# Performance work log

Measured on AMD Instinct MI355X. Metric: run time of the kernel, lower is better.

The kernel has to match this reference:

```python
import jax, jax.numpy as jnp
import numpy as np

N_NODES = 100000
N_EDGES = 1600000
D_IN = 128
H1 = 128           # hidden_channels
H2 = int(H1 * 0.6) # 76, per int(hidden_channels * 0.6)
D_OUT = 64


def setup_inputs() -> dict:
    key = jax.random.key(0)
    ks = jax.random.split(key, 12)
    def lin(k, fan_in, fan_out):
        # torch Linear default init: U(-1/sqrt(fan_in), 1/sqrt(fan_in)); stored as [in, out]
        bound = 1.0 / np.sqrt(fan_in)
        return jax.random.uniform(k, (fan_in, fan_out), jnp.float32, -bound, bound)
    x = jax.random.normal(ks[0], (N_NODES, D_IN), jnp.float32)
    edge_index = jax.random.randint(ks[1], (2, N_EDGES), 0, N_NODES, dtype=jnp.int64)
    return {
        "x": x,
        "edge_index": edge_index,
        "Wl1": lin(ks[2], D_IN, H1),  "Wr1": lin(ks[3], D_IN, H1),
        "b1": jnp.zeros((H1,), jnp.float32),
        "Wl2": lin(ks[4], H1, H2),    "Wr2": lin(ks[5], H1, H2),
        "b2": jnp.zeros((H2,), jnp.float32),
        "Wl3": lin(ks[6], H2, D_OUT), "Wr3": lin(ks[7], H2, D_OUT),
        "b3": jnp.zeros((D_OUT,), jnp.float32),
    }


def reference(x, edge_index, Wl1, Wr1, b1, Wl2, Wr2, b2, Wl3, Wr3, b3):
    src, dst = edge_index[0], edge_index[1]
    n = x.shape[0]
    # in-degree of each target node (mean aggregation denominator), clamped to 1
    deg = jax.ops.segment_sum(jnp.ones_like(src, dtype=x.dtype), dst, num_segments=n)
    inv_deg = (1.0 / jnp.maximum(deg, 1.0))[:, None]

    def sage(h, Wl, Wr, b):
        # gather source features, scatter-add to targets, mean, then dual linear
        agg = jax.ops.segment_sum(h[src], dst, num_segments=n) * inv_deg
        return agg @ Wl + h @ Wr + b  # lin_l(mean_j x_j) + lin_r(x_i) + bias

    h = jax.nn.relu(sage(x, Wl1, Wr1, b1))
    h = jax.nn.relu(sage(h, Wl2, Wr2, b2))
    return sage(h, Wl3, Wr3, b3)
```

## Files before the change

kernel.cpp:

```cpp
#include <hip/hip_runtime.h>
#include <hip/hip_bf16.h>
#include <cstdint>
#include <cstddef>


typedef __attribute__((ext_vector_type(8))) short bf16x8;
typedef __attribute__((ext_vector_type(4))) float f32x4;

__device__ __forceinline__ short f2bf(float f) {
  uint32_t u = __builtin_bit_cast(uint32_t, f);
  u += 0x7fffu + ((u >> 16) & 1u);
  return (short)(u >> 16);
}
__device__ __forceinline__ float bflo(uint32_t u) {
  union { uint32_t i; float f; } v; v.i = u << 16; return v.f;
}
__device__ __forceinline__ float bfhi(uint32_t u) {
  union { uint32_t i; float f; } v; v.i = u & 0xffff0000u; return v.f;
}
__device__ __forceinline__ uint32_t pkbf(float a, float b) {
  return (uint32_t)(uint16_t)f2bf(a) | ((uint32_t)(uint16_t)f2bf(b) << 16);
}

__global__ void k_detect(const int* __restrict__ ei, int* __restrict__ flag, int E) {
  int t = threadIdx.x;
  int stride = E / 4096; if (stride < 1) stride = 1;
  int found = 0;
  for (int i = t; i < 4096; i += 256) {
    long long e = (long long)i * stride;
    if (e < E && ei[2 * e + 1] != 0) found = 1;
  }
  if (found) atomicOr(flag, 1);
}

__device__ __forceinline__ int edge_val(const int* ei, int is64, size_t pos) {
  return is64 ? ei[2 * pos] : ei[pos];
}

#define GPART 256

__global__ __launch_bounds__(256)
void k_bhist(const int* __restrict__ ei, const int* __restrict__ flag,
             int* __restrict__ hist, int E, int NB, int CPB) {
  __shared__ int lh[1024];
  int g = blockIdx.x, t = threadIdx.x;
  for (int b = t; b < NB; b += 256) lh[b] = 0;
  __syncthreads();
  int is64 = (*flag == 0);
  int e0 = g * CPB, e1 = min(e0 + CPB, E);
  for (int e = e0 + t; e < e1; e += 256) {
    int d = edge_val(ei, is64, (size_t)E + e);
    atomicAdd(&lh[d >> 7], 1);
  }
  __syncthreads();
  for (int b = t; b < NB; b += 256) hist[(size_t)g * NB + b] = lh[b];
}

__global__ void k_csum(const int* __restrict__ hist, int* __restrict__ total,
                       int NB, int G) {
  int b = blockIdx.x, t = threadIdx.x;
  int s = 0;
  for (int g = t; g < G; g += 64) s += hist[(size_t)g * NB + b];
  for (int off = 32; off; off >>= 1) s += __shfl_down(s, off);
  if (t == 0) total[b] = s;
}

__global__ void k_bscan(const int* __restrict__ total, int* __restrict__ bbase,
                        int NB) {
  __shared__ int sh[1024];
  int t = threadIdx.x;
  int v = (t < NB) ? total[t] : 0;
  sh[t] = v; __syncthreads();
  for (int off = 1; off < 1024; off <<= 1) {
    int x = (t >= off) ? sh[t - off] : 0;
    __syncthreads();
    sh[t] += x;
    __syncthreads();
  }
  if (t < NB) bbase[t] = sh[t] - v;
  if (t == NB - 1) bbase[NB] = sh[t];
}

__global__ void k_coff(int* __restrict__ hist, const int* __restrict__ bbase,
                       int NB, int G) {
  int b = blockIdx.x, t = threadIdx.x;
  int carry = bbase[b];
  for (int g0 = 0; g0 < G; g0 += 64) {
    int v = hist[(size_t)(g0 + t) * NB + b];
    int incl = v;
    #pragma unroll
    for (int off = 1; off < 64; off <<= 1) {
      int x = __shfl_up(incl, off);
      if (t >= off) incl += x;
    }
    hist[(size_t)(g0 + t) * NB + b] = carry + incl - v;
    carry += __shfl(incl, 63);
  }
}

__global__ __launch_bounds__(256)
void k_bscatter(const int* __restrict__ ei, const int* __restrict__ flag,
                const int* __restrict__ off, uint32_t* __restrict__ staging,
                int E, int NB, int CPB) {
  __shared__ int lcur[1024];
  int g = blockIdx.x, t = threadIdx.x;
  for (int b = t; b < NB; b += 256) lcur[b] = off[(size_t)g * NB + b];
  __syncthreads();
  int is64 = (*flag == 0);
  int e0 = g * CPB, e1 = min(e0 + CPB, E);
  for (int e = e0 + t; e < e1; e += 256) {
    int s = edge_val(ei, is64, (size_t)e);
    int d = edge_val(ei, is64, (size_t)E + e);
    int p = atomicAdd(&lcur[d >> 7], 1);
    staging[p] = ((uint32_t)(d & 127) << 25) | (uint32_t)s;
  }
}

#define LDSCAP 12288
__global__ __launch_bounds__(256)
void k_bfinal(const uint32_t* __restrict__ staging, const int* __restrict__ bbase,
              int* __restrict__ row_start, int* __restrict__ sorted_src,
              int N, int NB, int E) {
  __shared__ uint32_t ent[LDSCAP];
  __shared__ int cnt[128];
  __shared__ int pre[128];
  int b = blockIdx.x, t = threadIdx.x;
  int base = bbase[b], sz = bbase[b + 1] - base;
  int n0 = b << 7;
  if (t < 128) cnt[t] = 0;
  __syncthreads();
  bool fit = (sz <= LDSCAP);
  if (fit) {
    for (int i = t; i < sz; i += 256) {
      uint32_t u = staging[base + i];
      ent[i] = u;
      atomicAdd(&cnt[u >> 25], 1);
    }
  } else {
    for (int i = t; i < sz; i += 256)
      atomicAdd(&cnt[staging[base + i] >> 25], 1);
  }
  __syncthreads();
  if (t < 128) pre[t] = cnt[t];
  __syncthreads();
  #pragma unroll
  for (int off = 1; off < 128; off <<= 1) {
    int x = (t < 128 && t >= off) ? pre[t - off] : 0;
    __syncthreads();
    if (t < 128) pre[t] += x;
    __syncthreads();
  }
  int nn = N - n0; if (nn > 128) nn = 128;
  if (t < 128) {
    int ex = pre[t] - cnt[t];
    if (t < nn) row_start[n0 + t] = base + ex;
    cnt[t] = ex;
  }
  if (b == NB - 1 && t == 0) row_start[N] = E;
  __syncthreads();
  if (fit) {
    for (int i = t; i < sz; i += 256) {
      uint32_t u = ent[i];
      int p = atomicAdd(&cnt[u >> 25], 1);
      sorted_src[base + p] = (int)(u & 0x1FFFFFFu);
    }
  } else {
    for (int i = t; i < sz; i += 256) {
      uint32_t u = staging[base + i];
      int p = atomicAdd(&cnt[u >> 25], 1);
      sorted_src[base + p] = (int)(u & 0x1FFFFFFu);
    }
  }
}

__global__ void k_wprep(const float* __restrict__ Wl, const float* __restrict__ Wr,
                        short* __restrict__ Wt, int K, int H, int Hp, int Kp, int NP) {
  int idx = blockIdx.x * 256 + threadIdx.x;
  if (idx >= NP * Kp) return;
  int c = idx / Kp, k = idx - c * Kp;
  float v = 0.f;
  if (k < K) {
    if (c < H) v = Wl[(size_t)k * H + c];
    else if (c >= Hp && c - Hp < H) v = Wr[(size_t)k * H + (c - Hp)];
  }
  Wt[idx] = f2bf(v);
}

template<int MODE, int NKS, int QBF16>
__global__ __launch_bounds__(256, 4)
void k_gemm2(const void* __restrict__ Av, const short* __restrict__ Wt,
             const float* __restrict__ bias, short* __restrict__ P,
             void* __restrict__ Qv, int M, int lda, int H, int Hp, int F) {
  const int Kp = NKS * 32;
  int t = threadIdx.x;
  int wv = t >> 6, lane = t & 63;
  int l16 = lane & 15, lk8 = (lane >> 4) * 8;
  int m0 = blockIdx.x * 64;
  int f0 = blockIdx.y * 8 + wv * 2;
  int nf = F - f0; nf = nf < 0 ? 0 : (nf > 2 ? 2 : nf);
  if (nf == 0) return;

  bf16x8 b[2][NKS];
  float4 bia[2];
  int cbase[2]; bool isPc[2]; bool cok[2];
  #pragma unroll
  for (int cf = 0; cf < 2; cf++) {
    int cfrag = f0 + cf;
    bool p = cfrag * 16 < Hp;
    int cb = cfrag * 16 + ((lane >> 4) << 2) - (p ? 0 : Hp);
    cbase[cf] = cb; isPc[cf] = p;
    cok[cf] = (cf < nf) && (cb < H);
    bia[cf] = make_float4(0.f, 0.f, 0.f, 0.f);
    if (cok[cf] && !p) bia[cf] = *(const float4*)(bias + cb);
    if (cf < nf) {
      const short* wp = Wt + (size_t)(cfrag * 16 + l16) * Kp + lk8;
      #pragma unroll
      for (int ks = 0; ks < NKS; ks++)
        b[cf][ks] = *(const bf16x8*)(wp + ks * 32);
    }
  }

  #pragma unroll
  for (int rf = 0; rf < 4; rf++) {
    int node = m0 + rf * 16 + l16;
    bool rok = node < M;
    bf16x8 a[NKS];
    if (MODE == 0) {
      const float* ap = (const float*)Av + (size_t)node * lda + lk8;
      #pragma unroll
      for (int ks = 0; ks < NKS; ks++) {
        if (rok) {
          float4 v0 = *(const float4*)(ap + ks * 32);
          float4 v1 = *(const float4*)(ap + ks * 32 + 4);
          bf16x8 r;
          r[0] = f2bf(v0.x); r[1] = f2bf(v0.y); r[2] = f2bf(v0.z); r[3] = f2bf(v0.w);
          r[4] = f2bf(v1.x); r[5] = f2bf(v1.y); r[6] = f2bf(v1.z); r[7] = f2bf(v1.w);
          a[ks] = r;
        } else {
          a[ks] = (bf16x8){0, 0, 0, 0, 0, 0, 0, 0};
        }
      }
    } else {
      const short* ap = (const short*)Av + (size_t)node * lda + lk8;
      #pragma unroll
      for (int ks = 0; ks < NKS; ks++)
        a[ks] = rok ? *(const bf16x8*)(ap + ks * 32)
                    : (bf16x8){0, 0, 0, 0, 0, 0, 0, 0};
    }

    f32x4 acc[2];
    acc[0] = (f32x4){0.f, 0.f, 0.f, 0.f};
    acc[1] = (f32x4){0.f, 0.f, 0.f, 0.f};
    #pragma unroll
    for (int ks = 0; ks < NKS; ks++) {
      #pragma unroll
      for (int cf = 0; cf < 2; cf++) {
        if (cf < nf)
          acc[cf] = __builtin_amdgcn_mfma_f32_16x16x32_bf16(b[cf][ks], a[ks], acc[cf], 0, 0, 0);
      }
    }

    if (rok) {
      #pragma unroll
      for (int cf = 0; cf < 2; cf++) {
        if (cok[cf]) {
          if (isPc[cf]) {
            uint2 pk;
            pk.x = pkbf(acc[cf][0], acc[cf][1]);
            pk.y = pkbf(acc[cf][2], acc[cf][3]);
            *(uint2*)(P + (size_t)node * H + cbase[cf]) = pk;
          } else if (QBF16) {
            uint2 pk;
            pk.x = pkbf(acc[cf][0] + bia[cf].x, acc[cf][1] + bia[cf].y);
            pk.y = pkbf(acc[cf][2] + bia[cf].z, acc[cf][3] + bia[cf].w);
            *(uint2*)((short*)Qv + (size_t)node * H + cbase[cf]) = pk;
          } else {
            float4 r;
            r.x = acc[cf][0] + bia[cf].x; r.y = acc[cf][1] + bia[cf].y;
            r.z = acc[cf][2] + bia[cf].z; r.w = acc[cf][3] + bia[cf].w;
            *(float4*)((float*)Qv + (size_t)node * H + cbase[cf]) = r;
          }
        }
      }
    }
  }
}

template<int RELU, int PACK, int OUTBF16, int QBF16>
__global__ __launch_bounds__(256)
void k_agg(const short* __restrict__ P, const void* Q,
           const int* __restrict__ rs, const int* __restrict__ srcs,
           void* out, int N, int H, int HSo) {
  int wave = threadIdx.x >> 6;
  int lane = threadIdx.x & 63;
  int node = blockIdx.x * 4 + wave;
  if (node >= N) return;
  int start = rs[node];
  int deg = rs[node + 1] - start;
  int c = lane * PACK;
  bool act = c < H;
  float a0 = 0.f, a1 = 0.f;
  const int* sp = srcs + start;

  for (int base = 0; base < deg; base += 64) {
    int cnt = deg - base; if (cnt > 64) cnt = 64;
    int myidx = (lane < cnt) ? sp[base + lane] : 0;
    int e = 0;
    int nfull = cnt & ~3;
    for (; e < nfull; e += 4) {
      int s0 = __shfl(myidx, e);
      int s1 = __shfl(myidx, e + 1);
      int s2 = __shfl(myidx, e + 2);
      int s3 = __shfl(myidx, e + 3);
      if (act) {
        if (PACK == 2) {
          uint32_t u0 = *(const uint32_t*)(P + (size_t)s0 * H + c);
          uint32_t u1 = *(const uint32_t*)(P + (size_t)s1 * H + c);
          uint32_t u2 = *(const uint32_t*)(P + (size_t)s2 * H + c);
          uint32_t u3 = *(const uint32_t*)(P + (size_t)s3 * H + c);
          a0 += bflo(u0); a1 += bfhi(u0);
          a0 += bflo(u1); a1 += bfhi(u1);
          a0 += bflo(u2); a1 += bfhi(u2);
          a0 += bflo(u3); a1 += bfhi(u3);
        } else {
          uint32_t u0 = *(const uint16_t*)(P + (size_t)s0 * H + c);
          uint32_t u1 = *(const uint16_t*)(P + (size_t)s1 * H + c);
          uint32_t u2 = *(const uint16_t*)(P + (size_t)s2 * H + c);
          uint32_t u3 = *(const uint16_t*)(P + (size_t)s3 * H + c);
          a0 += bflo(u0) + bflo(u1) + bflo(u2) + bflo(u3);
        }
      }
    }
    for (; e < cnt; ++e) {
      int s0 = __shfl(myidx, e);
      if (act) {
        if (PACK == 2) {
          uint32_t u0 = *(const uint32_t*)(P + (size_t)s0 * H + c);
          a0 += bflo(u0); a1 += bfhi(u0);
        } else {
          uint32_t u0 = *(const uint16_t*)(P + (size_t)s0 * H + c);
          a0 += bflo(u0);
        }
      }
    }
  }

  if (!act) return;
  float scale = 1.f / (float)(deg > 0 ? deg : 1);
  size_t oq = (size_t)node * H + c;
  size_t oo = (size_t)node * HSo + c;
  if (PACK == 2) {
    float q0, q1;
    if (QBF16) {
      uint32_t qu = *(const uint32_t*)((const short*)Q + oq);
      q0 = bflo(qu); q1 = bfhi(qu);
    } else {
      float2 q = *(const float2*)((const float*)Q + oq);
      q0 = q.x; q1 = q.y;
    }
    float v0 = a0 * scale + q0;
    float v1 = a1 * scale + q1;
    if (RELU) { v0 = fmaxf(v0, 0.f); v1 = fmaxf(v1, 0.f); }
    if (OUTBF16) {
      *(uint32_t*)((short*)out + oo) = pkbf(v0, v1);
    } else {
      float2 r; r.x = v0; r.y = v1;
      *(float2*)((float*)out + oo) = r;
    }
  } else {
    float q0;
    if (QBF16) q0 = bflo(*(const uint16_t*)((const short*)Q + oq));
    else       q0 = ((const float*)Q)[oq];
    float v0 = a0 * scale + q0;
    if (RELU) v0 = fmaxf(v0, 0.f);
    if (OUTBF16) ((short*)out)[oo] = f2bf(v0);
    else ((float*)out)[oo] = v0;
  }
}

extern "C" void kernel_launch(void* const* d_in, const int* in_sizes, int n_in,
                              void* d_out, int out_size, void* d_ws, size_t ws_size,
                              hipStream_t stream) {
  const float* x   = (const float*)d_in[0];
  const int*   ei  = (const int*)d_in[1];
  const float* Wl1 = (const float*)d_in[2];
  const float* Wr1 = (const float*)d_in[3];
  const float* b1  = (const float*)d_in[4];
  const float* Wl2 = (const float*)d_in[5];
  const float* Wr2 = (const float*)d_in[6];
  const float* b2  = (const float*)d_in[7];
  const float* Wl3 = (const float*)d_in[8];
  const float* Wr3 = (const float*)d_in[9];
  const float* b3  = (const float*)d_in[10];

  const int DIN = 128;
  const int N  = in_sizes[0] / DIN;
  const int E  = in_sizes[1] / 2;
  const int H1 = in_sizes[4];
  const int H2 = in_sizes[7];
  const int H3 = in_sizes[10];
  const int Hp1 = 128, Hp2 = 80, Hp3 = 64;
  const int Kp12 = 128, Kp3 = 96;
  const int NB = (N + 127) >> 7;
  const int G = GPART;
  const int CPB = (E + G - 1) / G;

  char* w = (char*)d_ws;
  auto alloc = [&](size_t bytes) {
    char* p = w;
    w += (bytes + 255) & ~(size_t)255;
    return p;
  };
  short* bufP  = (short*)alloc((size_t)N * 128 * 2);
  short* bufH1 = (short*)alloc((size_t)N * 128 * 2);
  short* bufH2 = (short*)alloc((size_t)N * 96 * 2);
  short* q1    = (short*)alloc((size_t)N * 128 * 2);
  short* q2    = (short*)alloc((size_t)N * 76 * 2);
  float* q3    = (float*)alloc((size_t)N * 64 * 4);
  short* Wt1   = (short*)alloc((size_t)256 * 128 * 2);
  short* Wt2   = (short*)alloc((size_t)160 * 128 * 2);
  short* Wt3   = (short*)alloc((size_t)128 * 96 * 2);
  int* row_start = (int*)alloc((size_t)(N + 1) * 4);
  int* hist      = (int*)alloc((size_t)G * NB * 4);
  int* total     = (int*)alloc((size_t)NB * 4);
  int* bbase     = (int*)alloc((size_t)(NB + 1) * 4);
  uint32_t* staging = (uint32_t*)alloc((size_t)E * 4);
  int* sorted    = (int*)alloc((size_t)E * 4);
  int* flag      = (int*)alloc(256);

  k_wprep<<<(256 * 128 + 255) / 256, 256, 0, stream>>>(Wl1, Wr1, Wt1, DIN, H1, Hp1, Kp12, 2 * Hp1);
  k_wprep<<<(160 * 128 + 255) / 256, 256, 0, stream>>>(Wl2, Wr2, Wt2, H1, H2, Hp2, Kp12, 2 * Hp2);
  k_wprep<<<(128 * 96 + 255) / 256, 256, 0, stream>>>(Wl3, Wr3, Wt3, H2, H3, Hp3, Kp3, 2 * Hp3);

  hipMemsetAsync(flag, 0, 4, stream);
  k_detect<<<1, 256, 0, stream>>>(ei, flag, E);
  k_bhist<<<G, 256, 0, stream>>>(ei, flag, hist, E, NB, CPB);
  k_csum<<<NB, 64, 0, stream>>>(hist, total, NB, G);
  k_bscan<<<1, 1024, 0, stream>>>(total, bbase, NB);
  k_coff<<<NB, 64, 0, stream>>>(hist, bbase, NB, G);
  k_bscatter<<<G, 256, 0, stream>>>(ei, flag, hist, staging, E, NB, CPB);
  k_bfinal<<<NB, 256, 0, stream>>>(staging, bbase, row_start, sorted, N, NB, E);

  int gx = (N + 63) / 64;
  int aggGrid = (N + 3) / 4;

  k_gemm2<0, 4, 1><<<dim3(gx, 2), 256, 0, stream>>>(x, Wt1, b1, bufP, q1, N, DIN, H1, Hp1, 16);
  k_agg<1, 2, 1, 1><<<aggGrid, 256, 0, stream>>>(bufP, q1, row_start, sorted, bufH1, N, H1, 128);

  k_gemm2<1, 4, 1><<<dim3(gx, 2), 256, 0, stream>>>(bufH1, Wt2, b2, bufP, q2, N, Kp12, H2, Hp2, 10);
  k_agg<1, 2, 1, 1><<<aggGrid, 256, 0, stream>>>(bufP, q2, row_start, sorted, bufH2, N, H2, 96);

  k_gemm2<1, 3, 0><<<dim3(gx, 1), 256, 0, stream>>>(bufH2, Wt3, b3, bufP, q3, N, Kp3, H3, Hp3, 8);
  k_agg<0, 1, 0, 0><<<aggGrid, 256, 0, stream>>>(bufP, q3, row_start, sorted, d_out, N, H3, 64);
}
```

Before: 363.3 us.

## Stage A tile in LDS and compute all output fragments per block

The GEMM kernel now loads each 64-row A tile once into shared memory, with coalesced loads and bf16 conversion done at staging. Each wave then computes up to four column fragments, so the old second grid dimension that re-read A from global memory goes away. The cost is more registers per wave for weight fragments and accumulators (launch bounds lowered to 3), an LDS footprint per block, and a barrier. The GEMMs are a small part of the pipeline next to the aggregation and sort steps.

```diff
diff --git a/kernel.cpp b/kernel.cpp
--- a/kernel.cpp
+++ b/kernel.cpp
@@ -186,99 +186,115 @@
   Wt[idx] = f2bf(v);
 }
 
-template<int MODE, int NKS, int QBF16>
-__global__ __launch_bounds__(256, 4)
-void k_gemm2(const void* __restrict__ Av, const short* __restrict__ Wt,
+template<int MODE, int NKS, int QBF16, int MAXCF>
+__global__ __launch_bounds__(256, 3)
+void k_gemm3(const void* __restrict__ Av, const short* __restrict__ Wt,
              const float* __restrict__ bias, short* __restrict__ P,
              void* __restrict__ Qv, int M, int lda, int H, int Hp, int F) {
-  const int Kp = NKS * 32;
+  constexpr int Kp = NKS * 32;
+  constexpr int PKv = Kp + 8;
+  __shared__ short As[64 * PKv];
   int t = threadIdx.x;
-  int wv = t >> 6, lane = t & 63;
+  int wv = __builtin_amdgcn_readfirstlane(t >> 6);
+  int lane = t & 63;
   int l16 = lane & 15, lk8 = (lane >> 4) * 8;
   int m0 = blockIdx.x * 64;
-  int f0 = blockIdx.y * 8 + wv * 2;
-  int nf = F - f0; nf = nf < 0 ? 0 : (nf > 2 ? 2 : nf);
-  if (nf == 0) return;
-
-  bf16x8 b[2][NKS];
-  float4 bia[2];
-  int cbase[2]; bool isPc[2]; bool cok[2];
+
+  if (MODE == 0) {
+    const float* A = (const float*)Av;
+    #pragma unroll
+    for (int i = 0; i < 8; i++) {
+      int c = t + i * 256;
+      int row = c >> 5, q = c & 31;
+      int gr = m0 + row;
+      float4 v = make_float4(0.f, 0.f, 0.f, 0.f);
+      if (gr < M) v = *(const float4*)(A + (size_t)gr * lda + q * 4);
+      uint2 pk; pk.x = pkbf(v.x, v.y); pk.y = pkbf(v.z, v.w);
+      *(uint2*)&As[row * PKv + q * 4] = pk;
+    }
+  } else {
+    const short* A = (const short*)Av;
+    constexpr int cpr = Kp / 8;
+    #pragma unroll
+    for (int i = 0; i < (64 * cpr) / 256; i++) {
+      int c = t + i * 256;
+      int row = c / cpr, q = c - row * cpr;
+      int gr = m0 + row;
+      uint4 v = make_uint4(0u, 0u, 0u, 0u);
+      if (gr < M) v = *(const uint4*)(A + (size_t)gr * lda + q * 8);
+      *(uint4*)&As[row * PKv + q * 8] = v;
+    }
+  }
+
+  bf16x8 b[MAXCF][NKS];
+  float4 bia[MAXCF];
+  int cbase[MAXCF];
+  bool isPc[MAXCF];
+  bool cok[MAXCF];
+  bool fragUse[MAXCF];
   #pragma unroll
-  for (int cf = 0; cf < 2; cf++) {
-    int cfrag = f0 + cf;
+  for (int i = 0; i < MAXCF; i++) {
+    int cfrag = wv + 4 * i;
+    fragUse[i] = cfrag < F;
     bool p = cfrag * 16 < Hp;
     int cb = cfrag * 16 + ((lane >> 4) << 2) - (p ? 0 : Hp);
-    cbase[cf] = cb; isPc[cf] = p;
-    cok[cf] = (cf < nf) && (cb < H);
-    bia[cf] = make_float4(0.f, 0.f, 0.f, 0.f);
-    if (cok[cf] && !p) bia[cf] = *(const float4*)(bias + cb);
-    if (cf < nf) {
+    cbase[i] = cb; isPc[i] = p;
+    cok[i] = fragUse[i] && (cb < H);
+    bia[i] = make_float4(0.f, 0.f, 0.f, 0.f);
+    if (cok[i] && !p) bia[i] = *(const float4*)(bias + cb);
+    if (fragUse[i]) {
       const short* wp = Wt + (size_t)(cfrag * 16 + l16) * Kp + lk8;
       #pragma unroll
       for (int ks = 0; ks < NKS; ks++)
-        b[cf][ks] = *(const bf16x8*)(wp + ks * 32);
-    }
-  }
+        b[i][ks] = *(const bf16x8*)(wp + ks * 32);
+    } else {
+      #pragma unroll
+      for (int ks = 0; ks < NKS; ks++)
+        b[i][ks] = (bf16x8){0, 0, 0, 0, 0, 0, 0, 0};
+    }
+  }
+
+  __syncthreads();
 
   #pragma unroll
   for (int rf = 0; rf < 4; rf++) {
-    int node = m0 + rf * 16 + l16;
-    bool rok = node < M;
     bf16x8 a[NKS];
-    if (MODE == 0) {
-      const float* ap = (const float*)Av + (size_t)node * lda + lk8;
-      #pragma unroll
-      for (int ks = 0; ks < NKS; ks++) {
-        if (rok) {
-          float4 v0 = *(const float4*)(ap + ks * 32);
-          float4 v1 = *(const float4*)(ap + ks * 32 + 4);
-          bf16x8 r;
-          r[0] = f2bf(v0.x); r[1] = f2bf(v0.y); r[2] = f2bf(v0.z); r[3] = f2bf(v0.w);
-          r[4] = f2bf(v1.x); r[5] = f2bf(v1.y); r[6] = f2bf(v1.z); r[7] = f2bf(v1.w);
-          a[ks] = r;
-        } else {
-          a[ks] = (bf16x8){0, 0, 0, 0, 0, 0, 0, 0};
-        }
-      }
-    } else {
-      const short* ap = (const short*)Av + (size_t)node * lda + lk8;
-      #pragma unroll
-      for (int ks = 0; ks < NKS; ks++)
-        a[ks] = rok ? *(const bf16x8*)(ap + ks * 32)
-                    : (bf16x8){0, 0, 0, 0, 0, 0, 0, 0};
-    }
-
-    f32x4 acc[2];
-    acc[0] = (f32x4){0.f, 0.f, 0.f, 0.f};
-    acc[1] = (f32x4){0.f, 0.f, 0.f, 0.f};
+    #pragma unroll
+    for (int ks = 0; ks < NKS; ks++)
+      a[ks] = *(const bf16x8*)&As[(rf * 16 + l16) * PKv + ks * 32 + lk8];
+
+    f32x4 acc[MAXCF];
+    #pragma unroll
+    for (int i = 0; i < MAXCF; i++) acc[i] = (f32x4){0.f, 0.f, 0.f, 0.f};
     #pragma unroll
     for (int ks = 0; ks < NKS; ks++) {
       #pragma unroll
-      for (int cf = 0; cf < 2; cf++) {
-        if (cf < nf)
-          acc[cf] = __builtin_amdgcn_mfma_f32_16x16x32_bf16(b[cf][ks], a[ks], acc[cf], 0, 0, 0);
+      for (int i = 0; i < MAXCF; i++) {
+        if (fragUse[i])
+          acc[i] = __builtin_amdgcn_mfma_f32_16x16x32_bf16(b[i][ks], a[ks], acc[i], 0, 0, 0);
       }
     }
 
-    if (rok) {
+    int node = m0 + rf * 16 + l16;
+    if (node < M) {
       #pragma unroll
-      for (int cf = 0; cf < 2; cf++) {
-        if (cok[cf]) {
-          if (isPc[cf]) {
+      for (int i = 0; i < MAXCF; i++) {
+        if (cok[i]) {
+          if (isPc[i]) {
             uint2 pk;
-            pk.x = pkbf(acc[cf][0], acc[cf][1]);
-            pk.y = pkbf(acc[cf][2], acc[cf][3]);
-            *(uint2*)(P + (size_t)node * H + cbase[cf]) = pk;
+            pk.x = pkbf(acc[i][0], acc[i][1]);
+            pk.y = pkbf(acc[i][2], acc[i][3]);
+            *(uint2*)(P + (size_t)node * H + cbase[i]) = pk;
           } else if (QBF16) {
             uint2 pk;
-            pk.x = pkbf(acc[cf][0] + bia[cf].x, acc[cf][1] + bia[cf].y);
-            pk.y = pkbf(acc[cf][2] + bia[cf].z, acc[cf][3] + bia[cf].w);
-            *(uint2*)((short*)Qv + (size_t)node * H + cbase[cf]) = pk;
+            pk.x = pkbf(acc[i][0] + bia[i].x, acc[i][1] + bia[i].y);
+            pk.y = pkbf(acc[i][2] + bia[i].z, acc[i][3] + bia[i].w);
+            *(uint2*)((short*)Qv + (size_t)node * H + cbase[i]) = pk;
           } else {
             float4 r;
-            r.x = acc[cf][0] + bia[cf].x; r.y = acc[cf][1] + bia[cf].y;
-            r.z = acc[cf][2] + bia[cf].z; r.w = acc[cf][3] + bia[cf].w;
-            *(float4*)((float*)Qv + (size_t)node * H + cbase[cf]) = r;
+            r.x = acc[i][0] + bia[i].x; r.y = acc[i][1] + bia[i].y;
+            r.z = acc[i][2] + bia[i].z; r.w = acc[i][3] + bia[i].w;
+            *(float4*)((float*)Qv + (size_t)node * H + cbase[i]) = r;
           }
         }
       }
@@ -444,12 +460,12 @@
   int gx = (N + 63) / 64;
   int aggGrid = (N + 3) / 4;
 
-  k_gemm2<0, 4, 1><<<dim3(gx, 2), 256, 0, stream>>>(x, Wt1, b1, bufP, q1, N, DIN, H1, Hp1, 16);
+  k_gemm3<0, 4, 1, 4><<<gx, 256, 0, stream>>>(x, Wt1, b1, bufP, q1, N, DIN, H1, Hp1, 16);
   k_agg<1, 2, 1, 1><<<aggGrid, 256, 0, stream>>>(bufP, q1, row_start, sorted, bufH1, N, H1, 128);
 
-  k_gemm2<1, 4, 1><<<dim3(gx, 2), 256, 0, stream>>>(bufH1, Wt2, b2, bufP, q2, N, Kp12, H2, Hp2, 10);
+  k_gemm3<1, 4, 1, 3><<<gx, 256, 0, stream>>>(bufH1, Wt2, b2, bufP, q2, N, Kp12, H2, Hp2, 10);
   k_agg<1, 2, 1, 1><<<aggGrid, 256, 0, stream>>>(bufP, q2, row_start, sorted, bufH2, N, H2, 96);
 
-  k_gemm2<1, 3, 0><<<dim3(gx, 1), 256, 0, stream>>>(bufH2, Wt3, b3, bufP, q3, N, Kp3, H3, Hp3, 8);
+  k_gemm3<1, 3, 0, 2><<<gx, 256, 0, stream>>>(bufH2, Wt3, b3, bufP, q3, N, Kp3, H3, Hp3, 8);
   k_agg<0, 1, 0, 0><<<aggGrid, 256, 0, stream>>>(bufP, q3, row_start, sorted, d_out, N, H3, 64);
 }
```

Measured after the change: 368.4 us. No clear change (+1.4%).

## Pre-convert x to bf16 and slim GEMM kernel registers for higher occupancy

Applied to the files above, without the earlier changes.

Adds a separate kernel that converts the fp32 input features to bf16 once, so the first GEMM reads bf16 like the later layers and the fp32 mode of the GEMM is removed. The GEMM now loads A fragments one k-step at a time, computes bias and column indices in the epilogue rather than holding them in registers, and raises the launch-bounds occupancy hint from 4 to 6. This lowers register pressure to allow more resident waves. In exchange it adds an extra kernel launch and a write and read of a 25 MB bf16 copy of x.

```diff
diff --git a/kernel.cpp b/kernel.cpp
--- a/kernel.cpp
+++ b/kernel.cpp
@@ -20,6 +20,18 @@
 }
 __device__ __forceinline__ uint32_t pkbf(float a, float b) {
   return (uint32_t)(uint16_t)f2bf(a) | ((uint32_t)(uint16_t)f2bf(b) << 16);
+}
+
+__global__ __launch_bounds__(256)
+void k_cvt(const float* __restrict__ x, short* __restrict__ xb, int n8) {
+  int i = blockIdx.x * 256 + threadIdx.x;
+  if (i >= n8) return;
+  const float4* p = (const float4*)x + (size_t)i * 2;
+  float4 v0 = p[0], v1 = p[1];
+  uint4 o;
+  o.x = pkbf(v0.x, v0.y); o.y = pkbf(v0.z, v0.w);
+  o.z = pkbf(v1.x, v1.y); o.w = pkbf(v1.z, v1.w);
+  ((uint4*)xb)[i] = o;
 }
 
 __global__ void k_detect(const int* __restrict__ ei, int* __restrict__ flag, int E) {
@@ -186,9 +198,9 @@
   Wt[idx] = f2bf(v);
 }
 
-template<int MODE, int NKS, int QBF16>
-__global__ __launch_bounds__(256, 4)
-void k_gemm2(const void* __restrict__ Av, const short* __restrict__ Wt,
+template<int NKS, int QBF16>
+__global__ __launch_bounds__(256, 6)
+void k_gemm5(const short* __restrict__ A, const short* __restrict__ Wt,
              const float* __restrict__ bias, short* __restrict__ P,
              void* __restrict__ Qv, int M, int lda, int H, int Hp, int F) {
   const int Kp = NKS * 32;
@@ -201,19 +213,10 @@
   if (nf == 0) return;
 
   bf16x8 b[2][NKS];
-  float4 bia[2];
-  int cbase[2]; bool isPc[2]; bool cok[2];
   #pragma unroll
   for (int cf = 0; cf < 2; cf++) {
-    int cfrag = f0 + cf;
-    bool p = cfrag * 16 < Hp;
-    int cb = cfrag * 16 + ((lane >> 4) << 2) - (p ? 0 : Hp);
-    cbase[cf] = cb; isPc[cf] = p;
-    cok[cf] = (cf < nf) && (cb < H);
-    bia[cf] = make_float4(0.f, 0.f, 0.f, 0.f);
-    if (cok[cf] && !p) bia[cf] = *(const float4*)(bias + cb);
     if (cf < nf) {
-      const short* wp = Wt + (size_t)(cfrag * 16 + l16) * Kp + lk8;
+      const short* wp = Wt + (size_t)((f0 + cf) * 16 + l16) * Kp + lk8;
       #pragma unroll
       for (int ks = 0; ks < NKS; ks++)
         b[cf][ks] = *(const bf16x8*)(wp + ks * 32);
@@ -224,62 +227,44 @@
   for (int rf = 0; rf < 4; rf++) {
     int node = m0 + rf * 16 + l16;
     bool rok = node < M;
-    bf16x8 a[NKS];
-    if (MODE == 0) {
-      const float* ap = (const float*)Av + (size_t)node * lda + lk8;
-      #pragma unroll
-      for (int ks = 0; ks < NKS; ks++) {
-        if (rok) {
-          float4 v0 = *(const float4*)(ap + ks * 32);
-          float4 v1 = *(const float4*)(ap + ks * 32 + 4);
-          bf16x8 r;
-          r[0] = f2bf(v0.x); r[1] = f2bf(v0.y); r[2] = f2bf(v0.z); r[3] = f2bf(v0.w);
-          r[4] = f2bf(v1.x); r[5] = f2bf(v1.y); r[6] = f2bf(v1.z); r[7] = f2bf(v1.w);
-          a[ks] = r;
-        } else {
-          a[ks] = (bf16x8){0, 0, 0, 0, 0, 0, 0, 0};
-        }
-      }
-    } else {
-      const short* ap = (const short*)Av + (size_t)node * lda + lk8;
-      #pragma unroll
-      for (int ks = 0; ks < NKS; ks++)
-        a[ks] = rok ? *(const bf16x8*)(ap + ks * 32)
-                    : (bf16x8){0, 0, 0, 0, 0, 0, 0, 0};
-    }
-
+    const short* ap = A + (size_t)node * lda + lk8;
     f32x4 acc[2];
     acc[0] = (f32x4){0.f, 0.f, 0.f, 0.f};
     acc[1] = (f32x4){0.f, 0.f, 0.f, 0.f};
     #pragma unroll
     for (int ks = 0; ks < NKS; ks++) {
-      #pragma unroll
-      for (int cf = 0; cf < 2; cf++) {
-        if (cf < nf)
-          acc[cf] = __builtin_amdgcn_mfma_f32_16x16x32_bf16(b[cf][ks], a[ks], acc[cf], 0, 0, 0);
-      }
-    }
-
-    if (rok) {
-      #pragma unroll
-      for (int cf = 0; cf < 2; cf++) {
-        if (cok[cf]) {
-          if (isPc[cf]) {
-            uint2 pk;
-            pk.x = pkbf(acc[cf][0], acc[cf][1]);
-            pk.y = pkbf(acc[cf][2], acc[cf][3]);
-            *(uint2*)(P + (size_t)node * H + cbase[cf]) = pk;
-          } else if (QBF16) {
-            uint2 pk;
-            pk.x = pkbf(acc[cf][0] + bia[cf].x, acc[cf][1] + bia[cf].y);
-            pk.y = pkbf(acc[cf][2] + bia[cf].z, acc[cf][3] + bia[cf].w);
-            *(uint2*)((short*)Qv + (size_t)node * H + cbase[cf]) = pk;
-          } else {
-            float4 r;
-            r.x = acc[cf][0] + bia[cf].x; r.y = acc[cf][1] + bia[cf].y;
-            r.z = acc[cf][2] + bia[cf].z; r.w = acc[cf][3] + bia[cf].w;
-            *(float4*)((float*)Qv + (size_t)node * H + cbase[cf]) = r;
-          }
+      bf16x8 a = rok ? *(const bf16x8*)(ap + ks * 32)
+                     : (bf16x8){0, 0, 0, 0, 0, 0, 0, 0};
+      acc[0] = __builtin_amdgcn_mfma_f32_16x16x32_bf16(b[0][ks], a, acc[0], 0, 0, 0);
+      if (nf == 2)
+        acc[1] = __builtin_amdgcn_mfma_f32_16x16x32_bf16(b[1][ks], a, acc[1], 0, 0, 0);
+    }
+
+    if (!rok) continue;
+    #pragma unroll
+    for (int cf = 0; cf < 2; cf++) {
+      if (cf >= nf) continue;
+      int cfrag = f0 + cf;
+      bool p = cfrag * 16 < Hp;
+      int cb = cfrag * 16 + ((lane >> 4) << 2) - (p ? 0 : Hp);
+      if (cb >= H) continue;
+      if (p) {
+        uint2 pk;
+        pk.x = pkbf(acc[cf][0], acc[cf][1]);
+        pk.y = pkbf(acc[cf][2], acc[cf][3]);
+        *(uint2*)(P + (size_t)node * H + cb) = pk;
+      } else {
+        float4 bi = *(const float4*)(bias + cb);
+        if (QBF16) {
+          uint2 pk;
+          pk.x = pkbf(acc[cf][0] + bi.x, acc[cf][1] + bi.y);
+          pk.y = pkbf(acc[cf][2] + bi.z, acc[cf][3] + bi.w);
+          *(uint2*)((short*)Qv + (size_t)node * H + cb) = pk;
+        } else {
+          float4 r;
+          r.x = acc[cf][0] + bi.x; r.y = acc[cf][1] + bi.y;
+          r.z = acc[cf][2] + bi.z; r.w = acc[cf][3] + bi.w;
+          *(float4*)((float*)Qv + (size_t)node * H + cb) = r;
         }
       }
     }
@@ -411,6 +396,7 @@
     w += (bytes + 255) & ~(size_t)255;
     return p;
   };
+  short* xb    = (short*)alloc((size_t)N * 128 * 2);
   short* bufP  = (short*)alloc((size_t)N * 128 * 2);
   short* bufH1 = (short*)alloc((size_t)N * 128 * 2);
   short* bufH2 = (short*)alloc((size_t)N * 96 * 2);
@@ -428,6 +414,8 @@
   int* sorted    = (int*)alloc((size_t)E * 4);
   int* flag      = (int*)alloc(256);
 
+  int n8 = N * DIN / 8;
+  k_cvt<<<(n8 + 255) / 256, 256, 0, stream>>>(x, xb, n8);
   k_wprep<<<(256 * 128 + 255) / 256, 256, 0, stream>>>(Wl1, Wr1, Wt1, DIN, H1, Hp1, Kp12, 2 * Hp1);
   k_wprep<<<(160 * 128 + 255) / 256, 256, 0, stream>>>(Wl2, Wr2, Wt2, H1, H2, Hp2, Kp12, 2 * Hp2);
   k_wprep<<<(128 * 96 + 255) / 256, 256, 0, stream>>>(Wl3, Wr3, Wt3, H2, H3, Hp3, Kp3, 2 * Hp3);
@@ -444,12 +432,12 @@
   int gx = (N + 63) / 64;
   int aggGrid = (N + 3) / 4;
 
-  k_gemm2<0, 4, 1><<<dim3(gx, 2), 256, 0, stream>>>(x, Wt1, b1, bufP, q1, N, DIN, H1, Hp1, 16);
+  k_gemm5<4, 1><<<dim3(gx, 2), 256, 0, stream>>>(xb, Wt1, b1, bufP, q1, N, 128, H1, Hp1, 16);
   k_agg<1, 2, 1, 1><<<aggGrid, 256, 0, stream>>>(bufP, q1, row_start, sorted, bufH1, N, H1, 128);
 
-  k_gemm2<1, 4, 1><<<dim3(gx, 2), 256, 0, stream>>>(bufH1, Wt2, b2, bufP, q2, N, Kp12, H2, Hp2, 10);
+  k_gemm5<4, 1><<<dim3(gx, 2), 256, 0, stream>>>(bufH1, Wt2, b2, bufP, q2, N, 128, H2, Hp2, 10);
   k_agg<1, 2, 1, 1><<<aggGrid, 256, 0, stream>>>(bufP, q2, row_start, sorted, bufH2, N, H2, 96);
 
-  k_gemm2<1, 3, 0><<<dim3(gx, 1), 256, 0, stream>>>(bufH2, Wt3, b3, bufP, q3, N, Kp3, H3, Hp3, 8);
+  k_gemm5<3, 0><<<dim3(gx, 1), 256, 0, stream>>>(bufH2, Wt3, b3, bufP, q3, N, 96, H3, Hp3, 8);
   k_agg<0, 1, 0, 0><<<aggGrid, 256, 0, stream>>>(bufP, q3, row_start, sorted, d_out, N, H3, 64);
 }
```

Result: slower. 379.1 us (+4.3%).
